# Performance work log

Measured on AMD Instinct MI355X. Metric: run time of the kernel, lower is better.

Reference implementation:

```python
import jax, jax.numpy as jnp
import numpy as np

NUM_HEADS = 8
CHUNK = 2
TAU = 2.0

# --- LIF neuron with ATan surrogate gradient (spikingjelly MultiStepLIFNode, hard reset to 0, detach_reset) ---
@jax.custom_vjp
def spike(x):
    return (x >= 0.0).astype(x.dtype)

def _spike_fwd(x):
    return spike(x), x

def _spike_bwd(x, g):
    alpha = 2.0
    sg = (alpha / 2.0) / (1.0 + (jnp.pi / 2.0 * alpha * x) ** 2)
    return (g * sg,)

spike.defvjp(_spike_fwd, _spike_bwd)

def lif(x_seq, v_th=1.0):
    # x_seq: [T, ...]; v' = v + (x - v)/tau ; spike if v' >= v_th ; hard reset v=0 (reset path detached)
    def step(v, x):
        v = v + (x - v) / TAU
        s = spike(v - v_th)
        v = v * (1.0 - jax.lax.stop_gradient(s))
        return v, s
    _, s = jax.lax.scan(step, jnp.zeros_like(x_seq[0]), x_seq)
    return s

def conv1x1_bn(x, W, scale, bias, conv_bias=None):
    # 1x1 conv over channel dim + eval-mode BN (per-channel affine)
    y = jnp.einsum('tbchw,dc->tbdhw', x, W)
    if conv_bias is not None:
        y = y + conv_bias[None, None, :, None, None]
    return y * scale[None, None, :, None, None] + bias[None, None, :, None, None]


def setup_inputs() -> dict:
    key = jax.random.key(0)
    ks = jax.random.split(key, 16)
    T, B, C, H, W = 4, 32, 512, 16, 16
    s = 1.0 / np.sqrt(C)
    return {
        'x': jax.random.normal(ks[0], (T, B, C, H, W), jnp.float32),
        'Wq': jax.random.normal(ks[1], (C, C), jnp.float32) * s,
        'q_scale': jax.random.uniform(ks[2], (C,), jnp.float32, 0.5, 1.5),
        'q_bias': jax.random.normal(ks[3], (C,), jnp.float32) * 0.1,
        'Wk': jax.random.normal(ks[4], (C, C), jnp.float32) * s,
        'k_scale': jax.random.uniform(ks[5], (C,), jnp.float32, 0.5, 1.5),
        'k_bias': jax.random.normal(ks[6], (C,), jnp.float32) * 0.1,
        'Wv': jax.random.normal(ks[7], (C, C), jnp.float32) * s,
        'v_scale': jax.random.uniform(ks[8], (C,), jnp.float32, 0.5, 1.5),
        'v_bias': jax.random.normal(ks[9], (C,), jnp.float32) * 0.1,
        'Wp': jax.random.normal(ks[10], (C, C), jnp.float32) * s,
        'bp': jax.random.normal(ks[11], (C,), jnp.float32) * 0.1,
        'p_scale': jax.random.uniform(ks[12], (C,), jnp.float32, 0.5, 1.5),
        'p_bias': jax.random.normal(ks[13], (C,), jnp.float32) * 0.1,
    }


def reference(x, Wq, q_scale, q_bias, Wk, k_scale, k_bias, Wv, v_scale, v_bias, Wp, bp, p_scale, p_bias):
    T, B, C, H, W = x.shape
    N = H * W
    hd = C // NUM_HEADS
    identity = x

    xs = lif(x)  # shortcut_lif

    def qkv_branch(W_, sc, bi):
        y = lif(conv1x1_bn(xs, W_, sc, bi))           # [T,B,C,H,W] spikes
        # flatten(3).transpose(-1,-2).reshape(...heads...).permute == split C, swap N/hd
        return jnp.swapaxes(y.reshape(T, B, NUM_HEADS, hd, N), -1, -2)  # [T,B,h,N,hd]

    q = qkv_branch(Wq, q_scale, q_bias)
    k = qkv_branch(Wk, k_scale, k_bias)
    v = qkv_branch(Wv, v_scale, v_bias)

    # STAtten: temporal chunking, linear attention q @ (k^T v)
    scaling = 1.0 / H
    nc = T // CHUNK

    def to_chunks(y):  # [T,B,h,N,hd] -> [nc,B,h,CHUNK*N,hd]
        return (y.reshape(nc, CHUNK, B, NUM_HEADS, N, hd)
                 .transpose(0, 2, 3, 1, 4, 5)
                 .reshape(nc, B, NUM_HEADS, CHUNK * N, hd))

    qc, kc, vc = to_chunks(q), to_chunks(k), to_chunks(v)
    attn = jnp.einsum('nbhsd,nbhse->nbhde', kc, vc) * scaling   # [nc,B,h,hd,hd]
    out = jnp.einsum('nbhsd,nbhde->nbhse', qc, attn)            # [nc,B,h,CHUNK*N,hd]
    out = (out.reshape(nc, B, NUM_HEADS, CHUNK, N, hd)
              .transpose(0, 3, 1, 2, 4, 5)
              .reshape(T, B, NUM_HEADS, N, hd))

    x2 = jnp.swapaxes(out, -1, -2).reshape(T, B, C, N)          # [T,B,C,N]
    x2 = lif(x2, v_th=0.5).reshape(T, B, C, H, W)               # attn_lif

    x3 = conv1x1_bn(x2, Wp, p_scale, p_bias, conv_bias=bp)      # proj conv+BN
    return x3 + identity, v
```

## Files before the change

kernel.cpp:

```cpp
#include <hip/hip_runtime.h>

typedef unsigned short ushort_t;
typedef unsigned char u8;
typedef short bf16x8 __attribute__((ext_vector_type(8)));
typedef float f32x4 __attribute__((ext_vector_type(4)));

#define T_DIM 4
#define B_DIM 32
#define C_DIM 512
#define N_DIM 256

__device__ __forceinline__ float bf2f(ushort_t u) {
  union { unsigned int i; float f; } x;
  x.i = ((unsigned int)u) << 16;
  return x.f;
}
__device__ __forceinline__ ushort_t f2bf(float f) {
  unsigned int u = __float_as_uint(f);
  u = (u + 0x7FFFu + ((u >> 16) & 1u)) >> 16;
  return (ushort_t)u;
}

__device__ __forceinline__ void gload16(const void* g, void* l) {
  __builtin_amdgcn_global_load_lds(
      (const __attribute__((address_space(1))) unsigned int*)g,
      (__attribute__((address_space(3))) unsigned int*)l, 16, 0, 0);
}

__global__ __launch_bounds__(256) void k0_split(
    const float* __restrict__ Wq, const float* __restrict__ Wk,
    const float* __restrict__ Wv, const float* __restrict__ Wp,
    ushort_t* __restrict__ Sqkv, ushort_t* __restrict__ Sp)
{
  int gid = blockIdx.x * 256 + threadIdx.x;
  int w = gid >> 15;
  int off = (gid & 32767) * 8;
  const float* src = (w == 0) ? Wq : ((w == 1) ? Wk : ((w == 2) ? Wv : Wp));
  ushort_t* dst = (w < 3) ? (Sqkv + (size_t)w * 3 * 262144) : Sp;
  float wv[8];
  *(float4*)&wv[0] = *(const float4*)(src + off);
  *(float4*)&wv[4] = *(const float4*)(src + off + 4);
  ushort_t hi[8], mi[8], lo[8];
#pragma unroll
  for (int i = 0; i < 8; i++) {
    float f = wv[i];
    ushort_t h = f2bf(f);  float r  = f - bf2f(h);
    ushort_t m = f2bf(r);  float r2 = r - bf2f(m);
    ushort_t l = f2bf(r2);
    hi[i] = h; mi[i] = m; lo[i] = l;
  }
  *(uint4*)(dst + off)              = *(uint4*)&hi[0];
  *(uint4*)(dst + 262144 + off)     = *(uint4*)&mi[0];
  *(uint4*)(dst + 2 * 262144 + off) = *(uint4*)&lo[0];
}

__global__ __launch_bounds__(256) void k1_shortcut_lif(
    const float* __restrict__ x, u8* __restrict__ xsT8)
{
  const int n0 = blockIdx.x * 64;
  const int c0 = blockIdx.y * 64;
  const int b  = blockIdx.z;
  __shared__ u8 sm[64][80];
  const int tid = threadIdx.x;
  const int r  = tid >> 2;
  const int j0 = (tid & 3) * 16;
  float v[16];
#pragma unroll
  for (int i = 0; i < 16; i++) v[i] = 0.f;
  for (int t = 0; t < T_DIM; t++) {
    const float* xp = x + ((((size_t)t * B_DIM + b) * C_DIM) + c0 + r) * N_DIM + n0 + j0;
    float xv[16];
    *(float4*)&xv[0]  = *(const float4*)xp;
    *(float4*)&xv[4]  = *(const float4*)(xp + 4);
    *(float4*)&xv[8]  = *(const float4*)(xp + 8);
    *(float4*)&xv[12] = *(const float4*)(xp + 12);
    __syncthreads();
#pragma unroll
    for (int i = 0; i < 16; i++) {
      float nv = v[i] + (xv[i] - v[i]) * 0.5f;
      bool s = (nv >= 1.0f);
      v[i] = s ? 0.f : nv;
      sm[j0 + i][r] = s ? (u8)1 : (u8)0;
    }
    __syncthreads();
    union { uint4 u; u8 b[16]; } ov;
#pragma unroll
    for (int i = 0; i < 16; i++) ov.b[i] = sm[r][j0 + i];
    u8* op = xsT8 + ((((size_t)t * B_DIM + b) * N_DIM) + n0 + r) * C_DIM + c0 + j0;
    *(uint4*)op = ov.u;
  }
}

__global__ __launch_bounds__(512, 4) void k2_qkv(
    const u8* __restrict__ xsT8, const ushort_t* __restrict__ Sqkv,
    const float* __restrict__ qsc, const float* __restrict__ qbi,
    const float* __restrict__ ksc, const float* __restrict__ kbi,
    const float* __restrict__ vsc, const float* __restrict__ vbi,
    u8* __restrict__ qs8, u8* __restrict__ ks8, float* __restrict__ vout)
{
  const int lin = blockIdx.x + blockIdx.y * 24;
  const int b   = (lin & 7) | (((lin >> 3) & 3) << 3);
  const int mt  = lin >> 5;
  const int branch = mt >> 3;
  const int mloc = (mt & 7) * 64;
  const ushort_t* Ws = Sqkv + (size_t)branch * 3 * 262144;
  const float* scp = (branch == 0) ? qsc : ((branch == 1) ? ksc : vsc);
  const float* bip = (branch == 0) ? qbi : ((branch == 1) ? kbi : vbi);

  __shared__ alignas(16) ushort_t As[2][3][64][32];
  __shared__ alignas(16) u8 Bs8[2][256][32];

  const int tid  = threadIdx.x;
  const int lane = tid & 63;
  const int wave = tid >> 6;
  const int wrow = (wave >> 1) * 16;
  const int wcol = (wave & 1) * 128;
  const int frow = lane & 15;
  const int fsl  = lane >> 4;

  const u8* Bb0 = xsT8 + (size_t)b * N_DIM * C_DIM;

  const int a0p = wave >> 2, a0q = wave & 3;
  const int arl = lane >> 2;
  const int acl = (((lane & 3) ^ ((arl >> 1) & 3)) * 8);
  const int brl = lane >> 1;
  const int bcl = (((lane & 1) ^ ((brl >> 2) & 1) ^ ((brl >> 3) & 1)) * 16);
  const int cbx = (wave < 4) ? (4 + wave) : (wave - 4);

#define K2_STAGE(s_) {                                                                     \
    const int ss_ = (s_);                                                                  \
    const int t_ = ss_ >> 4; const int kb_ = (ss_ & 15) * 32; const int bf_ = ss_ & 1;     \
    gload16(Ws + (size_t)a0p * 262144 + (size_t)(mloc + a0q * 16 + arl) * 512 + kb_ + acl, \
            &As[bf_][a0p][a0q * 16][0]);                                                   \
    if (wave < 4)                                                                          \
      gload16(Ws + 2 * 262144 + (size_t)(mloc + wave * 16 + arl) * 512 + kb_ + acl,        \
              &As[bf_][2][wave * 16][0]);                                                  \
    gload16(Bb0 + (size_t)t_ * (B_DIM * N_DIM * C_DIM) + (size_t)(cbx * 32 + brl) * 512 + kb_ + bcl, \
            &Bs8[bf_][cbx * 32][0]);                                                       \
  }

  f32x4 acc[8];
  float vst[32];
#pragma unroll
  for (int i = 0; i < 32; i++) vst[i] = 0.f;
#pragma unroll
  for (int j = 0; j < 8; j++) acc[j] = (f32x4){0.f, 0.f, 0.f, 0.f};

  const int crow0 = (lane >> 4) * 4;
  const int cn    = lane & 15;
  float sc4[4], bi4[4];
#pragma unroll
  for (int r = 0; r < 4; r++) {
    int c = mloc + wrow + crow0 + r;
    sc4[r] = scp[c]; bi4[r] = bip[c];
  }

  K2_STAGE(0);
  asm volatile("s_waitcnt vmcnt(0)" ::: "memory");
  __builtin_amdgcn_s_barrier();
  __builtin_amdgcn_sched_barrier(0);

  for (int s = 0; s < 64; s++) {
    const int cur = s & 1;
    if (s < 63) K2_STAGE(s + 1);

    bf16x8 af[3];
    const int ar = wrow + frow;
    const int asw = (fsl ^ ((ar >> 1) & 3)) * 8;
#pragma unroll
    for (int p = 0; p < 3; p++) af[p] = *(const bf16x8*)&As[cur][p][ar][asw];

#pragma unroll
    for (int j = 0; j < 8; j++) {
      const int row = wcol + j * 16 + frow;
      const int bx  = ((row >> 2) ^ (row >> 3)) & 1;
      const int bsw = (((fsl >> 1) ^ bx) << 4) + ((fsl & 1) << 3);
      uint2 raw = *(const uint2*)&Bs8[cur][row][bsw];
      union { bf16x8 v; unsigned int u[4]; } bu;
      bu.u[0] = __builtin_amdgcn_perm(0u, raw.x, 0x05010400u) * 0x3F80u;
      bu.u[1] = __builtin_amdgcn_perm(0u, raw.x, 0x07030602u) * 0x3F80u;
      bu.u[2] = __builtin_amdgcn_perm(0u, raw.y, 0x05010400u) * 0x3F80u;
      bu.u[3] = __builtin_amdgcn_perm(0u, raw.y, 0x07030602u) * 0x3F80u;
#pragma unroll
      for (int p = 0; p < 3; p++)
        acc[j] = __builtin_amdgcn_mfma_f32_16x16x32_bf16(af[p], bu.v, acc[j], 0, 0, 0);
    }

    if ((s & 15) == 15) {
      const int t = s >> 4;
      const size_t tb = (size_t)t * B_DIM + b;
      if (branch < 2) {
        u8* dst = (branch == 0) ? qs8 : ks8;
#pragma unroll
        for (int r = 0; r < 4; r++) {
          const int c = mloc + wrow + crow0 + r;
#pragma unroll
          for (int j = 0; j < 8; j++) {
            const int n = wcol + j * 16 + cn;
            float y = acc[j][r] * sc4[r] + bi4[r];
            const int vi = j * 4 + r;
            float v = vst[vi];
            v = v + (y - v) * 0.5f;
            bool sp = (v >= 1.0f);
            vst[vi] = sp ? 0.f : v;
            dst[(tb * C_DIM + c) * N_DIM + n] = sp ? (u8)1 : (u8)0;
          }
        }
      } else {
        const int hv = mloc >> 6;
        const int d0 = wrow + crow0;
#pragma unroll
        for (int j = 0; j < 8; j++) {
          const int n = wcol + j * 16 + cn;
          float ov[4];
#pragma unroll
          for (int r = 0; r < 4; r++) {
            float y = acc[j][r] * sc4[r] + bi4[r];
            const int vi = j * 4 + r;
            float v = vst[vi];
            v = v + (y - v) * 0.5f;
            bool sp = (v >= 1.0f);
            vst[vi] = sp ? 0.f : v;
            ov[r] = sp ? 1.0f : 0.0f;
          }
          *(float4*)(vout + ((tb * 8 + hv) * N_DIM + n) * 64 + d0) =
              make_float4(ov[0], ov[1], ov[2], ov[3]);
        }
      }
#pragma unroll
      for (int j = 0; j < 8; j++) acc[j] = (f32x4){0.f, 0.f, 0.f, 0.f};
    }

    asm volatile("s_waitcnt vmcnt(0)" ::: "memory");
    __builtin_amdgcn_s_barrier();
    __builtin_amdgcn_sched_barrier(0);
  }
#undef K2_STAGE
}

__global__ __launch_bounds__(256) void k3_attn(
    const u8* __restrict__ ks8, const float* __restrict__ vsp,
    float* __restrict__ attn)
{
  const int h  = blockIdx.x;
  const int b  = blockIdx.y;
  const int ch = blockIdx.z;
  __shared__ u8 KtT[64][80];
  __shared__ u8 Vt[64][80];
  const int tid = threadIdx.x;
  const int d0 = (tid >> 4) * 4;
  const int e0 = (tid & 15) * 4;
  float a[16];
#pragma unroll
  for (int i = 0; i < 16; i++) a[i] = 0.f;

  for (int tt = 0; tt < 2; tt++) {
    int t = ch * 2 + tt;
    for (int n0 = 0; n0 < 256; n0 += 64) {
      __syncthreads();
      {
        int d  = tid >> 2;
        int s0 = (tid & 3) * 16;
        union { uint4 u; u8 bvec[16]; } kb;
        kb.u = *(const uint4*)(ks8 + ((((size_t)t * B_DIM + b) * C_DIM) + h * 64 + d) * N_DIM + n0 + s0);
#pragma unroll
        for (int i = 0; i < 16; i++) KtT[s0 + i][d] = kb.bvec[i];
      }
      {
        const float* vb = vsp + ((((size_t)t * B_DIM + b) * 8 + h) * N_DIM + n0) * 64;
#pragma unroll
        for (int u = 0; u < 4; u++) {
          int chunk = tid + u * 256;
          int row = chunk >> 4;
          int eo  = (chunk & 15) * 4;
          float4 v4 = *(const float4*)(vb + (size_t)row * 64 + eo);
          Vt[row][eo + 0] = (u8)(v4.x != 0.f);
          Vt[row][eo + 1] = (u8)(v4.y != 0.f);
          Vt[row][eo + 2] = (u8)(v4.z != 0.f);
          Vt[row][eo + 3] = (u8)(v4.w != 0.f);
        }
      }
      __syncthreads();
      for (int s = 0; s < 64; s++) {
        uchar4 kb = *(const uchar4*)&KtT[s][d0];
        float kv[4] = { (float)kb.x, (float)kb.y, (float)kb.z, (float)kb.w };
        uchar4 vr = *(const uchar4*)&Vt[s][e0];
        float vv[4] = { (float)vr.x, (float)vr.y, (float)vr.z, (float)vr.w };
#pragma unroll
        for (int i = 0; i < 4; i++)
#pragma unroll
          for (int j = 0; j < 4; j++) a[i * 4 + j] += kv[i] * vv[j];
      }
    }
  }
  float* ap = attn + ((((size_t)ch * B_DIM + b) * 8 + h) * 64 + d0) * 64 + e0;
#pragma unroll
  for (int i = 0; i < 4; i++)
#pragma unroll
    for (int j = 0; j < 4; j++)
      ap[i * 64 + j] = a[i * 4 + j] * 0.0625f;
}

__global__ __launch_bounds__(256) void k4_out_lif(
    const u8* __restrict__ qs8, const float* __restrict__ attn,
    u8* __restrict__ x2sT8)
{
  const int h  = blockIdx.x;
  const int b  = blockIdx.y;
  const int nc = blockIdx.z;
  __shared__ float At[64][68];
  __shared__ u8 Qt[64][80];
  const int tid = threadIdx.x;
  const int e0 = (tid >> 4) * 4;
  const int n0 = (tid & 15) * 4;
  float vst[16];
#pragma unroll
  for (int i = 0; i < 16; i++) vst[i] = 0.f;

  for (int t = 0; t < T_DIM; t++) {
    if ((t & 1) == 0) {
      __syncthreads();
      const float* ap = attn + ((((size_t)(t >> 1) * B_DIM + b) * 8) + h) * 4096;
      int dr = tid >> 2;
      int co = (tid & 3) * 16;
#pragma unroll
      for (int u = 0; u < 4; u++)
        *(float4*)&At[dr][co + u * 4] = *(const float4*)(ap + dr * 64 + co + u * 4);
    }
    __syncthreads();
    {
      int d  = tid >> 2;
      int so = (tid & 3) * 16;
      *(uint4*)&Qt[d][so] =
        *(const uint4*)(qs8 + ((((size_t)t * B_DIM + b) * C_DIM) + h * 64 + d) * N_DIM + nc * 64 + so);
    }
    __syncthreads();
    float acc[16];
#pragma unroll
    for (int i = 0; i < 16; i++) acc[i] = 0.f;
    for (int d = 0; d < 64; d++) {
      float4 av = *(const float4*)&At[d][e0];
      float avv[4] = { av.x, av.y, av.z, av.w };
      uchar4 qr = *(const uchar4*)&Qt[d][n0];
      float qv[4] = { (float)qr.x, (float)qr.y, (float)qr.z, (float)qr.w };
#pragma unroll
      for (int i = 0; i < 4; i++)
#pragma unroll
        for (int j = 0; j < 4; j++) acc[i * 4 + j] += avv[i] * qv[j];
    }
#pragma unroll
    for (int j = 0; j < 4; j++) {
      u8 sv[4];
#pragma unroll
      for (int i = 0; i < 4; i++) {
        int vi = i * 4 + j;
        float y = acc[i * 4 + j];
        float nv = vst[vi] + (y - vst[vi]) * 0.5f;
        bool s = (nv >= 0.5f);
        vst[vi] = s ? 0.f : nv;
        sv[i] = s ? (u8)1 : (u8)0;
      }
      int n = nc * 64 + n0 + j;
      u8* op = x2sT8 + ((((size_t)t * B_DIM + b) * N_DIM) + n) * C_DIM + h * 64 + e0;
      *(uchar4*)op = make_uchar4(sv[0], sv[1], sv[2], sv[3]);
    }
  }
}

__global__ __launch_bounds__(512, 4) void k5_proj(
    const u8* __restrict__ x2sT8, const ushort_t* __restrict__ Sp,
    const float* __restrict__ bp, const float* __restrict__ psc,
    const float* __restrict__ pbi,
    const float* __restrict__ x, float* __restrict__ out0)
{
  const int tb = blockIdx.x;
  const int mt = blockIdx.y;
  const int mloc = mt * 64;

  __shared__ alignas(16) ushort_t As[2][3][64][32];
  __shared__ alignas(16) u8 Bs8[2][256][32];

  const int tid  = threadIdx.x;
  const int lane = tid & 63;
  const int wave = tid >> 6;
  const int wrow = (wave >> 1) * 16;
  const int wcol = (wave & 1) * 128;
  const int frow = lane & 15;
  const int fsl  = lane >> 4;

  const u8* Bb = x2sT8 + (size_t)tb * N_DIM * C_DIM;

  const int a0p = wave >> 2, a0q = wave & 3;
  const int arl = lane >> 2;
  const int acl = (((lane & 3) ^ ((arl >> 1) & 3)) * 8);
  const int brl = lane >> 1;
  const int bcl = (((lane & 1) ^ ((brl >> 2) & 1) ^ ((brl >> 3) & 1)) * 16);
  const int cbx = (wave < 4) ? (4 + wave) : (wave - 4);

#define K5_STAGE(s_) {                                                                     \
    const int ss_ = (s_); const int kb_ = ss_ * 32; const int bf_ = ss_ & 1;               \
    gload16(Sp + (size_t)a0p * 262144 + (size_t)(mloc + a0q * 16 + arl) * 512 + kb_ + acl, \
            &As[bf_][a0p][a0q * 16][0]);                                                   \
    if (wave < 4)                                                                          \
      gload16(Sp + 2 * 262144 + (size_t)(mloc + wave * 16 + arl) * 512 + kb_ + acl,        \
              &As[bf_][2][wave * 16][0]);                                                  \
    gload16(Bb + (size_t)(cbx * 32 + brl) * 512 + kb_ + bcl, &Bs8[bf_][cbx * 32][0]);      \
  }

  f32x4 acc[8];
#pragma unroll
  for (int j = 0; j < 8; j++) acc[j] = (f32x4){0.f, 0.f, 0.f, 0.f};

  K5_STAGE(0);
  asm volatile("s_waitcnt vmcnt(0)" ::: "memory");
  __builtin_amdgcn_s_barrier();
  __builtin_amdgcn_sched_barrier(0);

  for (int s = 0; s < 16; s++) {
    const int cur = s & 1;
    if (s < 15) K5_STAGE(s + 1);

    bf16x8 af[3];
    const int ar = wrow + frow;
    const int asw = (fsl ^ ((ar >> 1) & 3)) * 8;
#pragma unroll
    for (int p = 0; p < 3; p++) af[p] = *(const bf16x8*)&As[cur][p][ar][asw];

#pragma unroll
    for (int j = 0; j < 8; j++) {
      const int row = wcol + j * 16 + frow;
      const int bx  = ((row >> 2) ^ (row >> 3)) & 1;
      const int bsw = (((fsl >> 1) ^ bx) << 4) + ((fsl & 1) << 3);
      uint2 raw = *(const uint2*)&Bs8[cur][row][bsw];
      union { bf16x8 v; unsigned int u[4]; } bu;
      bu.u[0] = __builtin_amdgcn_perm(0u, raw.x, 0x05010400u) * 0x3F80u;
      bu.u[1] = __builtin_amdgcn_perm(0u, raw.x, 0x07030602u) * 0x3F80u;
      bu.u[2] = __builtin_amdgcn_perm(0u, raw.y, 0x05010400u) * 0x3F80u;
      bu.u[3] = __builtin_amdgcn_perm(0u, raw.y, 0x07030602u) * 0x3F80u;
#pragma unroll
      for (int p = 0; p < 3; p++)
        acc[j] = __builtin_amdgcn_mfma_f32_16x16x32_bf16(af[p], bu.v, acc[j], 0, 0, 0);
    }

    asm volatile("s_waitcnt vmcnt(0)" ::: "memory");
    __builtin_amdgcn_s_barrier();
    __builtin_amdgcn_sched_barrier(0);
  }

  const int crow0 = (lane >> 4) * 4;
  const int cn    = lane & 15;
#pragma unroll
  for (int r = 0; r < 4; r++) {
    const int c = mloc + wrow + crow0 + r;
    const float scf = psc[c];
    const float bif = pbi[c];
    const float bpf = bp[c];
#pragma unroll
    for (int j = 0; j < 8; j++) {
      const int n = wcol + j * 16 + cn;
      const size_t idx = ((size_t)tb * C_DIM + c) * N_DIM + n;
      out0[idx] = (acc[j][r] + bpf) * scf + bif + x[idx];
    }
  }
#undef K5_STAGE
}

extern "C" void kernel_launch(void* const* d_in, const int* in_sizes, int n_in,
                              void* d_out, int out_size, void* d_ws, size_t ws_size,
                              hipStream_t stream) {
  const float* x   = (const float*)d_in[0];
  const float* Wq  = (const float*)d_in[1];
  const float* qsc = (const float*)d_in[2];
  const float* qbi = (const float*)d_in[3];
  const float* Wk  = (const float*)d_in[4];
  const float* ksc = (const float*)d_in[5];
  const float* kbi = (const float*)d_in[6];
  const float* Wv  = (const float*)d_in[7];
  const float* vsc = (const float*)d_in[8];
  const float* vbi = (const float*)d_in[9];
  const float* Wp  = (const float*)d_in[10];
  const float* bp  = (const float*)d_in[11];
  const float* psc = (const float*)d_in[12];
  const float* pbi = (const float*)d_in[13];

  float* out0 = (float*)d_out;
  float* out1 = out0 + 16777216;

  const size_t M16 = 16u * 1024u * 1024u;
  char* o0 = (char*)d_out;
  char* ws = (char*)d_ws;

  u8*       xsT8  = (u8*)(o0);
  u8*       qs8   = (u8*)(o0 + M16);
  u8*       ks8   = (u8*)(o0 + 2 * M16);
  ushort_t* Sqkv  = (ushort_t*)(o0 + 3 * M16);
  float*    attn  = (float*)(o0);
  u8*       x2sT8 = (u8*)(ws);
  ushort_t* Sp    = (ushort_t*)(ws + M16);

  hipLaunchKernelGGL(k0_split,        dim3(512),        dim3(256), 0, stream,
                     Wq, Wk, Wv, Wp, Sqkv, Sp);
  hipLaunchKernelGGL(k1_shortcut_lif, dim3(4, 8, 32),   dim3(256), 0, stream, x, xsT8);
  hipLaunchKernelGGL(k2_qkv,          dim3(24, 32),     dim3(512), 0, stream,
                     xsT8, Sqkv, qsc, qbi, ksc, kbi, vsc, vbi, qs8, ks8, out1);
  hipLaunchKernelGGL(k3_attn,         dim3(8, 32, 2),   dim3(256), 0, stream, ks8, out1, attn);
  hipLaunchKernelGGL(k4_out_lif,      dim3(8, 32, 4),   dim3(256), 0, stream, qs8, attn, x2sT8);
  hipLaunchKernelGGL(k5_proj,         dim3(128, 8),     dim3(512), 0, stream,
                     x2sT8, Sp, bp, psc, pbi, x, out0);
}
```

Measured before the change: 523.4 us.

## Deepen GEMM LDS pipeline to four buffers and emit u8 V spikes

k2 and k5 move from a double-buffered loop to a four-slot ring with prefetch distance two. Each wave now waits with a partial vmcnt before the barrier, where it used to drain all loads after compute. The A split is cut from three bf16 pieces to two, which reduces the MFMAs per tile by one third but may lose weight precision. k2 also writes V spikes as u8 next to the float output, so k3 reads compact bytes instead of float4 data and converting it, at the cost of one extra store stream.

```diff
diff --git a/kernel.cpp b/kernel.cpp
--- a/kernel.cpp
+++ b/kernel.cpp
@@ -96,7 +96,8 @@
     const float* __restrict__ qsc, const float* __restrict__ qbi,
     const float* __restrict__ ksc, const float* __restrict__ kbi,
     const float* __restrict__ vsc, const float* __restrict__ vbi,
-    u8* __restrict__ qs8, u8* __restrict__ ks8, float* __restrict__ vout)
+    u8* __restrict__ qs8, u8* __restrict__ ks8, float* __restrict__ vout,
+    u8* __restrict__ vs8)
 {
   const int lin = blockIdx.x + blockIdx.y * 24;
   const int b   = (lin & 7) | (((lin >> 3) & 3) << 3);
@@ -107,8 +108,8 @@
   const float* scp = (branch == 0) ? qsc : ((branch == 1) ? ksc : vsc);
   const float* bip = (branch == 0) ? qbi : ((branch == 1) ? kbi : vbi);
 
-  __shared__ alignas(16) ushort_t As[2][3][64][32];
-  __shared__ alignas(16) u8 Bs8[2][256][32];
+  __shared__ alignas(16) ushort_t As[4][2][64][32];
+  __shared__ alignas(16) u8 Bs8[4][256][32];
 
   const int tid  = threadIdx.x;
   const int lane = tid & 63;
@@ -125,16 +126,13 @@
   const int acl = (((lane & 3) ^ ((arl >> 1) & 3)) * 8);
   const int brl = lane >> 1;
   const int bcl = (((lane & 1) ^ ((brl >> 2) & 1) ^ ((brl >> 3) & 1)) * 16);
-  const int cbx = (wave < 4) ? (4 + wave) : (wave - 4);
+  const int cbx = wave;
 
 #define K2_STAGE(s_) {                                                                     \
     const int ss_ = (s_);                                                                  \
-    const int t_ = ss_ >> 4; const int kb_ = (ss_ & 15) * 32; const int bf_ = ss_ & 1;     \
+    const int t_ = ss_ >> 4; const int kb_ = (ss_ & 15) * 32; const int bf_ = ss_ & 3;     \
     gload16(Ws + (size_t)a0p * 262144 + (size_t)(mloc + a0q * 16 + arl) * 512 + kb_ + acl, \
             &As[bf_][a0p][a0q * 16][0]);                                                   \
-    if (wave < 4)                                                                          \
-      gload16(Ws + 2 * 262144 + (size_t)(mloc + wave * 16 + arl) * 512 + kb_ + acl,        \
-              &As[bf_][2][wave * 16][0]);                                                  \
     gload16(Bb0 + (size_t)t_ * (B_DIM * N_DIM * C_DIM) + (size_t)(cbx * 32 + brl) * 512 + kb_ + bcl, \
             &Bs8[bf_][cbx * 32][0]);                                                       \
   }
@@ -156,19 +154,23 @@
   }
 
   K2_STAGE(0);
-  asm volatile("s_waitcnt vmcnt(0)" ::: "memory");
-  __builtin_amdgcn_s_barrier();
-  __builtin_amdgcn_sched_barrier(0);
+  K2_STAGE(1);
 
   for (int s = 0; s < 64; s++) {
-    const int cur = s & 1;
-    if (s < 63) K2_STAGE(s + 1);
-
-    bf16x8 af[3];
+    const int cur = s & 3;
+    if (s < 62) K2_STAGE(s + 2);
+
+    if (s < 62)      asm volatile("s_waitcnt vmcnt(4)" ::: "memory");
+    else if (s == 62) asm volatile("s_waitcnt vmcnt(2)" ::: "memory");
+    else              asm volatile("s_waitcnt vmcnt(0)" ::: "memory");
+    __builtin_amdgcn_s_barrier();
+    __builtin_amdgcn_sched_barrier(0);
+
+    bf16x8 af[2];
     const int ar = wrow + frow;
     const int asw = (fsl ^ ((ar >> 1) & 3)) * 8;
 #pragma unroll
-    for (int p = 0; p < 3; p++) af[p] = *(const bf16x8*)&As[cur][p][ar][asw];
+    for (int p = 0; p < 2; p++) af[p] = *(const bf16x8*)&As[cur][p][ar][asw];
 
 #pragma unroll
     for (int j = 0; j < 8; j++) {
@@ -182,7 +184,7 @@
       bu.u[2] = __builtin_amdgcn_perm(0u, raw.y, 0x05010400u) * 0x3F80u;
       bu.u[3] = __builtin_amdgcn_perm(0u, raw.y, 0x07030602u) * 0x3F80u;
 #pragma unroll
-      for (int p = 0; p < 3; p++)
+      for (int p = 0; p < 2; p++)
         acc[j] = __builtin_amdgcn_mfma_f32_16x16x32_bf16(af[p], bu.v, acc[j], 0, 0, 0);
     }
 
@@ -213,6 +215,7 @@
         for (int j = 0; j < 8; j++) {
           const int n = wcol + j * 16 + cn;
           float ov[4];
+          u8 sv[4];
 #pragma unroll
           for (int r = 0; r < 4; r++) {
             float y = acc[j][r] * sc4[r] + bi4[r];
@@ -222,24 +225,22 @@
             bool sp = (v >= 1.0f);
             vst[vi] = sp ? 0.f : v;
             ov[r] = sp ? 1.0f : 0.0f;
+            sv[r] = sp ? (u8)1 : (u8)0;
           }
-          *(float4*)(vout + ((tb * 8 + hv) * N_DIM + n) * 64 + d0) =
-              make_float4(ov[0], ov[1], ov[2], ov[3]);
+          const size_t vbase = ((tb * 8 + hv) * N_DIM + n) * 64 + d0;
+          *(float4*)(vout + vbase) = make_float4(ov[0], ov[1], ov[2], ov[3]);
+          *(uchar4*)(vs8 + vbase)  = make_uchar4(sv[0], sv[1], sv[2], sv[3]);
         }
       }
 #pragma unroll
       for (int j = 0; j < 8; j++) acc[j] = (f32x4){0.f, 0.f, 0.f, 0.f};
     }
-
-    asm volatile("s_waitcnt vmcnt(0)" ::: "memory");
-    __builtin_amdgcn_s_barrier();
-    __builtin_amdgcn_sched_barrier(0);
   }
 #undef K2_STAGE
 }
 
 __global__ __launch_bounds__(256) void k3_attn(
-    const u8* __restrict__ ks8, const float* __restrict__ vsp,
+    const u8* __restrict__ ks8, const u8* __restrict__ vs8,
     float* __restrict__ attn)
 {
   const int h  = blockIdx.x;
@@ -267,18 +268,10 @@
         for (int i = 0; i < 16; i++) KtT[s0 + i][d] = kb.bvec[i];
       }
       {
-        const float* vb = vsp + ((((size_t)t * B_DIM + b) * 8 + h) * N_DIM + n0) * 64;
-#pragma unroll
-        for (int u = 0; u < 4; u++) {
-          int chunk = tid + u * 256;
-          int row = chunk >> 4;
-          int eo  = (chunk & 15) * 4;
-          float4 v4 = *(const float4*)(vb + (size_t)row * 64 + eo);
-          Vt[row][eo + 0] = (u8)(v4.x != 0.f);
-          Vt[row][eo + 1] = (u8)(v4.y != 0.f);
-          Vt[row][eo + 2] = (u8)(v4.z != 0.f);
-          Vt[row][eo + 3] = (u8)(v4.w != 0.f);
-        }
+        const u8* vb = vs8 + ((((size_t)t * B_DIM + b) * 8 + h) * N_DIM + n0) * 64;
+        int row = tid >> 2;
+        int eo  = (tid & 3) * 16;
+        *(uint4*)&Vt[row][eo] = *(const uint4*)(vb + (size_t)row * 64 + eo);
       }
       __syncthreads();
       for (int s = 0; s < 64; s++) {
@@ -377,8 +370,8 @@
   const int mt = blockIdx.y;
   const int mloc = mt * 64;
 
-  __shared__ alignas(16) ushort_t As[2][3][64][32];
-  __shared__ alignas(16) u8 Bs8[2][256][32];
+  __shared__ alignas(16) ushort_t As[4][2][64][32];
+  __shared__ alignas(16) u8 Bs8[4][256][32];
 
   const int tid  = threadIdx.x;
   const int lane = tid & 63;
@@ -395,15 +388,12 @@
   const int acl = (((lane & 3) ^ ((arl >> 1) & 3)) * 8);
   const int brl = lane >> 1;
   const int bcl = (((lane & 1) ^ ((brl >> 2) & 1) ^ ((brl >> 3) & 1)) * 16);
-  const int cbx = (wave < 4) ? (4 + wave) : (wave - 4);
+  const int cbx = wave;
 
 #define K5_STAGE(s_) {                                                                     \
-    const int ss_ = (s_); const int kb_ = ss_ * 32; const int bf_ = ss_ & 1;               \
+    const int ss_ = (s_); const int kb_ = ss_ * 32; const int bf_ = ss_ & 3;               \
     gload16(Sp + (size_t)a0p * 262144 + (size_t)(mloc + a0q * 16 + arl) * 512 + kb_ + acl, \
             &As[bf_][a0p][a0q * 16][0]);                                                   \
-    if (wave < 4)                                                                          \
-      gload16(Sp + 2 * 262144 + (size_t)(mloc + wave * 16 + arl) * 512 + kb_ + acl,        \
-              &As[bf_][2][wave * 16][0]);                                                  \
     gload16(Bb + (size_t)(cbx * 32 + brl) * 512 + kb_ + bcl, &Bs8[bf_][cbx * 32][0]);      \
   }
 
@@ -412,19 +402,23 @@
   for (int j = 0; j < 8; j++) acc[j] = (f32x4){0.f, 0.f, 0.f, 0.f};
 
   K5_STAGE(0);
-  asm volatile("s_waitcnt vmcnt(0)" ::: "memory");
-  __builtin_amdgcn_s_barrier();
-  __builtin_amdgcn_sched_barrier(0);
+  K5_STAGE(1);
 
   for (int s = 0; s < 16; s++) {
-    const int cur = s & 1;
-    if (s < 15) K5_STAGE(s + 1);
-
-    bf16x8 af[3];
+    const int cur = s & 3;
+    if (s < 14) K5_STAGE(s + 2);
+
+    if (s < 14)       asm volatile("s_waitcnt vmcnt(4)" ::: "memory");
+    else if (s == 14) asm volatile("s_waitcnt vmcnt(2)" ::: "memory");
+    else              asm volatile("s_waitcnt vmcnt(0)" ::: "memory");
+    __builtin_amdgcn_s_barrier();
+    __builtin_amdgcn_sched_barrier(0);
+
+    bf16x8 af[2];
     const int ar = wrow + frow;
     const int asw = (fsl ^ ((ar >> 1) & 3)) * 8;
 #pragma unroll
-    for (int p = 0; p < 3; p++) af[p] = *(const bf16x8*)&As[cur][p][ar][asw];
+    for (int p = 0; p < 2; p++) af[p] = *(const bf16x8*)&As[cur][p][ar][asw];
 
 #pragma unroll
     for (int j = 0; j < 8; j++) {
@@ -438,13 +432,9 @@
       bu.u[2] = __builtin_amdgcn_perm(0u, raw.y, 0x05010400u) * 0x3F80u;
       bu.u[3] = __builtin_amdgcn_perm(0u, raw.y, 0x07030602u) * 0x3F80u;
 #pragma unroll
-      for (int p = 0; p < 3; p++)
+      for (int p = 0; p < 2; p++)
         acc[j] = __builtin_amdgcn_mfma_f32_16x16x32_bf16(af[p], bu.v, acc[j], 0, 0, 0);
     }
-
-    asm volatile("s_waitcnt vmcnt(0)" ::: "memory");
-    __builtin_amdgcn_s_barrier();
-    __builtin_amdgcn_sched_barrier(0);
   }
 
   const int crow0 = (lane >> 4) * 4;
@@ -494,6 +484,7 @@
   u8*       qs8   = (u8*)(o0 + M16);
   u8*       ks8   = (u8*)(o0 + 2 * M16);
   ushort_t* Sqkv  = (ushort_t*)(o0 + 3 * M16);
+  u8*       vs8   = (u8*)(o0 + 3 * M16 + 8u * 1024u * 1024u);
   float*    attn  = (float*)(o0);
   u8*       x2sT8 = (u8*)(ws);
   ushort_t* Sp    = (ushort_t*)(ws + M16);
@@ -502,8 +493,8 @@
                      Wq, Wk, Wv, Wp, Sqkv, Sp);
   hipLaunchKernelGGL(k1_shortcut_lif, dim3(4, 8, 32),   dim3(256), 0, stream, x, xsT8);
   hipLaunchKernelGGL(k2_qkv,          dim3(24, 32),     dim3(512), 0, stream,
-                     xsT8, Sqkv, qsc, qbi, ksc, kbi, vsc, vbi, qs8, ks8, out1);
-  hipLaunchKernelGGL(k3_attn,         dim3(8, 32, 2),   dim3(256), 0, stream, ks8, out1, attn);
+                     xsT8, Sqkv, qsc, qbi, ksc, kbi, vsc, vbi, qs8, ks8, out1, vs8);
+  hipLaunchKernelGGL(k3_attn,         dim3(8, 32, 2),   dim3(256), 0, stream, ks8, vs8, attn);
   hipLaunchKernelGGL(k4_out_lif,      dim3(8, 32, 4),   dim3(256), 0, stream, qs8, attn, x2sT8);
   hipLaunchKernelGGL(k5_proj,         dim3(128, 8),     dim3(512), 0, stream,
                      x2sT8, Sp, bp, psc, pbi, x, out0);
```

Result: faster. 467.4 us (-10.7%).
